# Kernel tuning notes

Measured on AMD Instinct MI355X. Metric: run time of the kernel, lower is better.

## Reference

```python
import jax, jax.numpy as jnp
import numpy as np

N_NODES = 50000
N_EDGES = 800000
HIDDEN = 128
EPS = 1e-5


def _layernorm(x, g, b):
    m = jnp.mean(x, axis=-1, keepdims=True)
    v = jnp.var(x, axis=-1, keepdims=True)
    return (x - m) / jnp.sqrt(v + EPS) * g + b


def _batchnorm(x, g, b):
    # training-mode BatchNorm1d: stats over the node (batch) axis, biased var
    m = jnp.mean(x, axis=0, keepdims=True)
    v = jnp.var(x, axis=0, keepdims=True)
    return (x - m) / jnp.sqrt(v + EPS) * g + b


def _instnorm(x):
    # torch InstanceNorm1d on a 2D [N,C] input: unbatched (C,L) view ->
    # normalize each row over the feature axis, no affine params
    m = jnp.mean(x, axis=-1, keepdims=True)
    v = jnp.var(x, axis=-1, keepdims=True)
    return (x - m) / jnp.sqrt(v + EPS)


def _gcn_conv(x, W, b, row, col, norm, n):
    # PyG GCNConv: out[col] += norm * (x @ W)[row]; + bias
    xw = x @ W
    msgs = xw[row] * norm[:, None]          # [E+N, H]
    out = jax.ops.segment_sum(msgs, col, num_segments=n)
    return out + b


def setup_inputs() -> dict:
    key = jax.random.key(0)
    ks = jax.random.split(key, 12)
    H = HIDDEN
    x = jax.random.normal(ks[0], (N_NODES, 2), dtype=jnp.float32)
    edge_index = jax.random.randint(ks[1], (2, N_EDGES), 0, N_NODES, dtype=jnp.int64)

    def lin(k, fan_in, shape):
        bound = 1.0 / np.sqrt(fan_in)
        return jax.random.uniform(k, shape, jnp.float32, -bound, bound)

    inp = {
        "x": x,
        "edge_index": edge_index,
        "coord_W": lin(ks[2], 2, (2, H)),
        "coord_b": lin(ks[3], 2, (H,)),
        "ln_g": jnp.ones((H,), jnp.float32),
        "ln_b": jnp.zeros((H,), jnp.float32),
        "bn_g": jnp.ones((H,), jnp.float32),
        "bn_b": jnp.zeros((H,), jnp.float32),
        "W1": lin(ks[4], H, (H, H)),
        "b1": jnp.zeros((H,), jnp.float32),
        "W2": lin(ks[5], H, (H, H)),
        "b2": jnp.zeros((H,), jnp.float32),
        "W3": lin(ks[6], H, (H, H)),
        "b3": jnp.zeros((H,), jnp.float32),
        "fc1_W": lin(ks[7], H, (H, 32)),
        "fc1_b": lin(ks[8], H, (32,)),
        "fc2_W": lin(ks[9], 32, (32, 2)),
        "fc2_b": lin(ks[10], 32, (2,)),
    }
    return inp


def reference(x, edge_index, coord_W, coord_b, ln_g, ln_b, bn_g, bn_b,
              W1, b1, W2, b2, W3, b3, fc1_W, fc1_b, fc2_W, fc2_b):
    n = x.shape[0]
    loop = jnp.arange(n, dtype=edge_index.dtype)
    row = jnp.concatenate([edge_index[0], loop])
    col = jnp.concatenate([edge_index[1], loop])
    deg = jax.ops.segment_sum(jnp.ones_like(col, dtype=x.dtype), col, num_segments=n)
    dinv = 1.0 / jnp.sqrt(deg)              # deg >= 1 thanks to self-loops
    norm = dinv[row] * dinv[col]

    h = jax.nn.relu(x @ coord_W + coord_b)
    h = _layernorm(h, ln_g, ln_b)

    for W, b in ((W1, b1), (W2, b2), (W3, b3)):
        identity = h
        h = jax.nn.relu(_gcn_conv(h, W, b, row, col, norm, n))
        h = _batchnorm(h, bn_g, bn_b)
        h = _instnorm(h + identity)

    h = jax.nn.relu(h @ fc1_W + fc1_b)
    return jnp.tanh(h @ fc2_W + fc2_b)
```

## Files before the change

kernel.cpp:

```cpp
#include <hip/hip_runtime.h>
#include <hip/hip_bf16.h>
#include <hip/hip_fp16.h>
#include <stdint.h>

#define NN 50000
#define NE 800000
#define HD 128
#define EPSN 1e-5f
#define CAP 1152000

typedef __hip_bfloat16 bf16;
typedef __attribute__((ext_vector_type(8))) _Float16 half8;
typedef __attribute__((ext_vector_type(4))) float f32x4;

__device__ __forceinline__ float us2f(unsigned short u) { return __uint_as_float((uint32_t)u << 16); }
__device__ __forceinline__ ushort f2us(float f) {
    bf16 b = __float2bfloat16(f);
    return *reinterpret_cast<ushort*>(&b);
}
__device__ __forceinline__ ushort f2h(float f) {
    __half h = __float2half(f);
    return *reinterpret_cast<ushort*>(&h);
}
__device__ __forceinline__ float h2f(ushort u) {
    __half h = *reinterpret_cast<__half*>(&u);
    return __half2float(h);
}

__device__ __forceinline__ void cvt8(float4 v, float* o) {
    uint32_t a = __float_as_uint(v.x), b = __float_as_uint(v.y);
    uint32_t c = __float_as_uint(v.z), d = __float_as_uint(v.w);
    o[0] = h2f((ushort)(a & 0xffff)); o[1] = h2f((ushort)(a >> 16));
    o[2] = h2f((ushort)(b & 0xffff)); o[3] = h2f((ushort)(b >> 16));
    o[4] = h2f((ushort)(c & 0xffff)); o[5] = h2f((ushort)(c >> 16));
    o[6] = h2f((ushort)(d & 0xffff)); o[7] = h2f((ushort)(d >> 16));
}

#define O_X    0
#define O_CW   100000
#define O_CB   100256
#define O_LNG  100384
#define O_LNB  100512
#define O_BNG  100640
#define O_BNB  100768
#define O_W1   100896
#define O_B1   117280
#define O_W2   117408
#define O_B2   133792
#define O_W3   133920
#define O_B3   150304
#define O_F1W  150432
#define O_F1B  154528
#define O_F2W  154560
#define O_F2B  154624
#define O_TOT  154626

struct Ptrs { const void* p[17]; };

__device__ const int SEG_OFF[18] = {O_X, O_CW, O_CB, O_LNG, O_LNB, O_BNG, O_BNB,
                                    O_W1, O_B1, O_W2, O_B2, O_W3, O_B3,
                                    O_F1W, O_F1B, O_F2W, O_F2B, O_TOT};

__device__ __forceinline__ int eidx(const int* __restrict__ ei, int isL, int which, int e) {
    size_t base = (size_t)which * NE + e;
    return isL ? ei[2 * base] : ei[base];
}

__global__ void k_detect(const int* __restrict__ ei, const ushort* __restrict__ cw,
                         int* __restrict__ flags) {
    int t = threadIdx.x;
    int v = ei[2 * t + 1] | ei[1000000 + 2 * t + 1];
    int bad = 0;
    if (t < 128) {
        float val = us2f(cw[2 * t]);
        bad = !(fabsf(val) <= 1.0f);
    }
    for (int o = 32; o; o >>= 1) { v |= __shfl_xor(v, o); bad |= __shfl_xor(bad, o); }
    __shared__ int sv[4], sb[4];
    if ((t & 63) == 0) { sv[t >> 6] = v; sb[t >> 6] = bad; }
    __syncthreads();
    if (t == 0) {
        flags[0] = ((sv[0] | sv[1] | sv[2] | sv[3]) == 0) ? 1 : 0;
        flags[1] = ((sb[0] | sb[1] | sb[2] | sb[3]) == 0) ? 1 : 0;
    }
}

__global__ void k_conv(Ptrs ptrs, const int* __restrict__ flags, float* __restrict__ cp) {
    int i = blockIdx.x * 256 + threadIdx.x;
    if (i >= O_TOT) return;
    int s = 0;
    while (i >= SEG_OFF[s + 1]) s++;
    int local = i - SEG_OFF[s];
    const void* src = ptrs.p[s];
    cp[i] = flags[1] ? us2f(((const ushort*)src)[local]) : ((const float*)src)[local];
}

__global__ void k_wconv(const float* __restrict__ cp, _Float16* __restrict__ wt) {
    int e = blockIdx.x * 256 + threadIdx.x;
    if (e >= 3 * HD * HD) return;
    int mat = e >> 14, idx = e & (HD * HD - 1);
    int k = idx >> 7, n = idx & 127;
    const float* W = cp + (mat == 0 ? O_W1 : (mat == 1 ? O_W2 : O_W3));
    wt[mat * HD * HD + n * HD + k] = (_Float16)W[k * HD + n];
}


__global__ void k_init(int* __restrict__ deg, float* __restrict__ stats,
                       int* __restrict__ cursor) {
    int i = blockIdx.x * 256 + threadIdx.x;
    if (i < NN) deg[i] = 1;
    if (i < 3072) stats[i] = 0.f;
    if (i == 0) *cursor = 0;
}

__global__ void k_deg(const int* __restrict__ ei, const int* __restrict__ flags,
                      int* __restrict__ deg) {
    int e = blockIdx.x * 256 + threadIdx.x;
    if (e < NE) atomicAdd(&deg[eidx(ei, flags[0], 1, e)], 1);
}

__global__ void k_dinv_alloc(const int* __restrict__ deg, float* __restrict__ dinv,
                             int* __restrict__ startA, int* __restrict__ curA,
                             int* __restrict__ cursor, int2* __restrict__ srw) {
    int i = blockIdx.x * 256 + threadIdx.x;
    if (i < NN) {
        int d = deg[i];
        dinv[i] = rsqrtf((float)d);
        int cnt = d - 1;
        int cpad = (cnt + 7) & ~7;
        int s = atomicAdd(cursor, cpad);
        startA[i] = s;
        curA[i] = s;
        for (int p = s + cnt; p < s + cpad; p++) srw[p] = make_int2(0, 0);
    }
}

__global__ void k_fill(const int* __restrict__ ei, const int* __restrict__ flags,
                       const float* __restrict__ dinv, int* __restrict__ curA,
                       int2* __restrict__ srw) {
    int e = blockIdx.x * 256 + threadIdx.x;
    if (e >= NE) return;
    int isL = flags[0];
    int r = eidx(ei, isL, 0, e);
    int c = eidx(ei, isL, 1, e);
    int p = atomicAdd(&curA[c], 1);
    srw[p] = make_int2(r << 4, __float_as_int(dinv[r] * dinv[c]));
}


__global__ void k_embed(const float* __restrict__ cp, float* __restrict__ h) {
    int node = (blockIdx.x * 256 + threadIdx.x) >> 6;
    int lane = threadIdx.x & 63;
    if (node >= NN) return;
    const float* X = cp + O_X;
    const float* CW = cp + O_CW;
    const float* CB = cp + O_CB;
    const float* LG = cp + O_LNG;
    const float* LB = cp + O_LNB;
    float x0 = X[node * 2], x1 = X[node * 2 + 1];
    int f0 = lane, f1 = lane + 64;
    float v0 = fmaxf(0.f, x0 * CW[f0] + x1 * CW[HD + f0] + CB[f0]);
    float v1 = fmaxf(0.f, x0 * CW[f1] + x1 * CW[HD + f1] + CB[f1]);
    float s = v0 + v1, q = v0 * v0 + v1 * v1;
    for (int o = 32; o; o >>= 1) { s += __shfl_xor(s, o); q += __shfl_xor(q, o); }
    float m = s * (1.f / HD);
    float var = q * (1.f / HD) - m * m;
    float r = rsqrtf(var + EPSN);
    h[(size_t)node * HD + f0] = (v0 - m) * r * LG[f0] + LB[f0];
    h[(size_t)node * HD + f1] = (v1 - m) * r * LG[f1] + LB[f1];
}


__device__ __forceinline__ void mfma_tile(const _Float16* hl, const _Float16* __restrict__ wt,
                                          ushort* __restrict__ t0h, int nodeBase, int t) {
    int w = t >> 6, l = t & 63;
    int m16 = l & 15;
    int kg = l >> 4;
    int node0 = w * 16;
    half8 a[4];
#pragma unroll
    for (int kc = 0; kc < 4; kc++) {
        int nd = node0 + m16;
        int c16 = kc * 4 + kg;
        int chunk = nd * 16 + (c16 ^ (nd & 7));
        a[kc] = *(const half8*)(hl + chunk * 8);
    }
    f32x4 acc[8];
#pragma unroll
    for (int nt = 0; nt < 8; nt++) acc[nt] = (f32x4){0.f, 0.f, 0.f, 0.f};
#pragma unroll
    for (int nt = 0; nt < 8; nt++) {
        const half8* bp = (const half8*)(wt + (size_t)(nt * 16 + m16) * HD);
#pragma unroll
        for (int kc = 0; kc < 4; kc++) {
            acc[nt] = __builtin_amdgcn_mfma_f32_16x16x32_f16(a[kc], bp[kc * 4 + kg],
                                                             acc[nt], 0, 0, 0);
        }
    }
    int ndb = nodeBase + node0 + kg * 4;
#pragma unroll
    for (int rr = 0; rr < 4; rr++) {
        int nd = ndb + rr;
        if (nd < NN) {
#pragma unroll
            for (int nt = 0; nt < 8; nt++) {
                t0h[(size_t)nd * HD + nt * 16 + m16] = f2h(acc[nt][rr]);
            }
        }
    }
}


__global__ __launch_bounds__(256) void k_gemm(const float* __restrict__ h,
                                              const _Float16* __restrict__ wt,
                                              ushort* __restrict__ t0h) {
    __shared__ _Float16 hl[64 * HD];
    int t = threadIdx.x;
    int nodeBase = blockIdx.x * 64;
    const float4* h4 = (const float4*)h;
#pragma unroll
    for (int r = 0; r < 4; r++) {
        int cid = r * 256 + t;
        int node = cid >> 4;
        int c16 = cid & 15;
        int n = nodeBase + node;
        float4 u0 = make_float4(0.f, 0.f, 0.f, 0.f), u1 = u0;
        if (n < NN) {
            u0 = h4[(size_t)n * 32 + c16 * 2];
            u1 = h4[(size_t)n * 32 + c16 * 2 + 1];
        }
        half8 v;
        v[0] = (_Float16)u0.x; v[1] = (_Float16)u0.y;
        v[2] = (_Float16)u0.z; v[3] = (_Float16)u0.w;
        v[4] = (_Float16)u1.x; v[5] = (_Float16)u1.y;
        v[6] = (_Float16)u1.z; v[7] = (_Float16)u1.w;
        int chunk = node * 16 + (c16 ^ (node & 7));
        *(half8*)(hl + chunk * 8) = v;
    }
    __syncthreads();
    mfma_tile(hl, wt, t0h, nodeBase, t);
}


__global__ __launch_bounds__(256) void k_gemm_fused(const float* __restrict__ agg,
                                                    const float* __restrict__ stats,
                                                    const float* __restrict__ bias,
                                                    const float* __restrict__ bng,
                                                    const float* __restrict__ bnb,
                                                    float* __restrict__ h,
                                                    const _Float16* __restrict__ wt,
                                                    ushort* __restrict__ t0h) {
    __shared__ _Float16 hl[64 * HD];
    __shared__ float scL[HD], shL[HD], bL[HD];
    int t = threadIdx.x;
    if (t < 128) {
        const float invN = 1.f / NN;
        float sv = stats[t] + stats[256 + t] + stats[512 + t] + stats[768 + t];
        float qv = stats[128 + t] + stats[384 + t] + stats[640 + t] + stats[896 + t];
        float m = sv * invN;
        float v = qv * invN - m * m;
        float sc = bng[t] * rsqrtf(v + EPSN);
        scL[t] = sc;
        shL[t] = bnb[t] - m * sc;
        bL[t] = bias[t];
    }
    __syncthreads();
    int nodeBase = blockIdx.x * 64;
    const float4* a4 = (const float4*)agg;
    float4* h4g = (float4*)h;
#pragma unroll
    for (int r = 0; r < 8; r++) {
        int idx = r * 256 + t;
        int node = idx >> 5;
        int c4 = idx & 31;
        int n = nodeBase + node;
        float4 u = make_float4(0.f, 0.f, 0.f, 0.f);
        if (n < NN) {
            float4 av = a4[(size_t)n * 32 + c4];
            float4 hv = h4g[(size_t)n * 32 + c4];
            int f = c4 * 4;
            float y0 = fmaxf(0.f, av.x + bL[f]);
            float y1 = fmaxf(0.f, av.y + bL[f + 1]);
            float y2 = fmaxf(0.f, av.z + bL[f + 2]);
            float y3 = fmaxf(0.f, av.w + bL[f + 3]);
            u.x = y0 * scL[f]     + shL[f]     + hv.x;
            u.y = y1 * scL[f + 1] + shL[f + 1] + hv.y;
            u.z = y2 * scL[f + 2] + shL[f + 2] + hv.z;
            u.w = y3 * scL[f + 3] + shL[f + 3] + hv.w;
        }
        float s = u.x + u.y + u.z + u.w;
        float q = u.x * u.x + u.y * u.y + u.z * u.z + u.w * u.w;
        for (int o = 16; o; o >>= 1) { s += __shfl_xor(s, o); q += __shfl_xor(q, o); }
        float m = s * (1.f / HD);
        float var = q * (1.f / HD) - m * m;
        float rr = rsqrtf(var + EPSN);
        u.x = (u.x - m) * rr; u.y = (u.y - m) * rr;
        u.z = (u.z - m) * rr; u.w = (u.w - m) * rr;
        if (n < NN) h4g[(size_t)n * 32 + c4] = u;
        ushort4 pk;
        pk.x = f2h(u.x); pk.y = f2h(u.y); pk.z = f2h(u.z); pk.w = f2h(u.w);
        int chunk = node * 16 + ((c4 >> 1) ^ (node & 7));
        *(ushort4*)((char*)hl + chunk * 16 + (c4 & 1) * 8) = pk;
    }
    __syncthreads();
    mfma_tile(hl, wt, t0h, nodeBase, t);
}


__global__ __launch_bounds__(256) void k_agg(const ushort* __restrict__ t0h,
                                             const int2* __restrict__ srw,
                                             const int* __restrict__ startA,
                                             const int* __restrict__ deg,
                                             const float* __restrict__ dinv,
                                             const float* __restrict__ bias,
                                             float* __restrict__ agg,
                                             float* __restrict__ stats) {
    int t = threadIdx.x;
    int w = t >> 6;
    int l = t & 63;
    int g = l >> 4;
    int k = l & 15;
    int l32 = l & 31;
    const float4* t04 = (const float4*)t0h;
    float4* agg4 = (float4*)agg;
    float bs[8];
    {
        const float4* b4 = (const float4*)bias;
        float4 u0 = b4[2 * k], u1 = b4[2 * k + 1];
        bs[0] = u0.x; bs[1] = u0.y; bs[2] = u0.z; bs[3] = u0.w;
        bs[4] = u1.x; bs[5] = u1.y; bs[6] = u1.z; bs[7] = u1.w;
    }
    float rs1[8], rs2[8];
#pragma unroll
    for (int m = 0; m < 8; m++) { rs1[m] = 0.f; rs2[m] = 0.f; }
    int stride = gridDim.x * 4;
    int i = blockIdx.x * 4 + w;
    int s = 0, nb = 0;
    float di = 0.f;
    if (i < NN) {
        s = startA[i];
        nb = (deg[i] - 1 + 7) & ~7;
        di = dinv[i];
    }
    while (i < NN) {
        float4 sv = t04[(size_t)i * 16 + k];
        int2 e = make_int2(0, 0);
        if (l32 < nb) e = srw[s + l32];
        int ex = e.x, ey = e.y;
        int nb4 = nb >> 2;
        float4 gg[8];
#define GATH(b) { int rv = __shfl(ex, 4 * (b) + g); \
                  gg[b] = t04[(size_t)(uint32_t)rv + k]; }
        if (nb4 > 0) { GATH(0) GATH(1) }
        if (nb4 > 2) { GATH(2) GATH(3) }
        if (nb4 > 4) { GATH(4) GATH(5) }
        if (nb4 > 6) { GATH(6) GATH(7) }
#undef GATH
        int inext = i + stride;
        int sN = 0, nbN = 0;
        float diN = 0.f;
        if (inext < NN) {
            sN = startA[inext];
            nbN = (deg[inext] - 1 + 7) & ~7;
            diN = dinv[inext];
        }
        float acc[8], c8[8];
        cvt8(sv, c8);
        float ws = (g == 0) ? di * di : 0.f;
#pragma unroll
        for (int m = 0; m < 8; m++) acc[m] = ws * c8[m];
#define ACCB(b) { float wv = __int_as_float(__shfl(ey, 4 * (b) + g)); \
                  float d8[8]; cvt8(gg[b], d8); \
                  _Pragma("unroll") \
                  for (int m = 0; m < 8; m++) acc[m] += wv * d8[m]; }
        if (nb4 > 0) { ACCB(0) ACCB(1) }
        if (nb4 > 2) { ACCB(2) ACCB(3) }
        if (nb4 > 4) { ACCB(4) ACCB(5) }
        if (nb4 > 6) { ACCB(6) ACCB(7) }
#undef ACCB
        for (int j = 32; j < nb; j += 32) {
            int2 e2 = make_int2(0, 0);
            if (j + l32 < nb) e2 = srw[s + j + l32];
            int ex2 = e2.x, ey2 = e2.y;
            int rem4 = (nb - j) >> 2;
            if (rem4 > 8) rem4 = 8;
            for (int b = 0; b < rem4; b += 2) {
                int r0 = __shfl(ex2, 4 * b + g);
                int r1 = __shfl(ex2, 4 * b + 4 + g);
                float4 g0 = t04[(size_t)(uint32_t)r0 + k];
                float4 g1 = t04[(size_t)(uint32_t)r1 + k];
                float w0 = __int_as_float(__shfl(ey2, 4 * b + g));
                float w1 = __int_as_float(__shfl(ey2, 4 * b + 4 + g));
                float d0[8], d1[8];
                cvt8(g0, d0); cvt8(g1, d1);
#pragma unroll
                for (int m = 0; m < 8; m++) acc[m] += w0 * d0[m] + w1 * d1[m];
            }
        }
#pragma unroll
        for (int m = 0; m < 8; m++) {
            acc[m] += __shfl_xor(acc[m], 16);
            acc[m] += __shfl_xor(acc[m], 32);
        }
        if (g == 0) {
            agg4[(size_t)i * 32 + 2 * k]     = make_float4(acc[0], acc[1], acc[2], acc[3]);
            agg4[(size_t)i * 32 + 2 * k + 1] = make_float4(acc[4], acc[5], acc[6], acc[7]);
        }
#pragma unroll
        for (int m = 0; m < 8; m++) {
            float y = fmaxf(0.f, acc[m] + bs[m]);
            rs1[m] += y;
            rs2[m] += y * y;
        }
        i = inext; s = sN; nb = nbN; di = diN;
    }
    __shared__ float s1[4][HD], s2[4][HD];
    if (l < 16) {
#pragma unroll
        for (int m = 0; m < 8; m++) {
            s1[w][k * 8 + m] = rs1[m];
            s2[w][k * 8 + m] = rs2[m];
        }
    }
    __syncthreads();
    float* st = stats + (blockIdx.x & 3) * 256;
    if (t < 128) {
        atomicAdd(&st[t], s1[0][t] + s1[1][t] + s1[2][t] + s1[3][t]);
    } else {
        int f = t - 128;
        atomicAdd(&st[128 + f], s2[0][f] + s2[1][f] + s2[2][f] + s2[3][f]);
    }
}


__global__ __launch_bounds__(256) void k_tail(const float* __restrict__ agg,
                                              const float* __restrict__ stats,
                                              const float* __restrict__ h,
                                              const float* __restrict__ cp,
                                              const int* __restrict__ flags,
                                              void* __restrict__ outv) {
    __shared__ float W1l[HD * 32];
    __shared__ float ub[4][HD];
    __shared__ float scT[HD], shT[HD], bT[HD];
    __shared__ float B1s[32], W2s[64], B2s[2];
    int t = threadIdx.x;
    const float4* f1w4 = (const float4*)(cp + O_F1W);
    float4* w14 = (float4*)W1l;
#pragma unroll
    for (int r = 0; r < 4; r++) w14[r * 256 + t] = f1w4[r * 256 + t];
    if (t < 32) B1s[t] = cp[O_F1B + t];
    if (t < 64) W2s[t] = cp[O_F2W + t];
    if (t < 2) B2s[t] = cp[O_F2B + t];
    if (t < 128) {
        const float invN = 1.f / NN;
        float sv = stats[t] + stats[256 + t] + stats[512 + t] + stats[768 + t];
        float qv = stats[128 + t] + stats[384 + t] + stats[640 + t] + stats[896 + t];
        float m = sv * invN;
        float v = qv * invN - m * m;
        float sc = cp[O_BNG + t] * rsqrtf(v + EPSN);
        scT[t] = sc;
        shT[t] = cp[O_BNB + t] - m * sc;
        bT[t] = cp[O_B3 + t];
    }
    __syncthreads();
    int isBf = flags[1];
    int w = t >> 6, l = t & 63;
    int f = l & 31, half = l >> 5;
    for (int base = blockIdx.x * 4; base < NN; base += gridDim.x * 4) {
        int node = base + w;
        if (node >= NN) continue;
        size_t o = (size_t)node * HD;
        float a0 = agg[o + l], a1 = agg[o + l + 64];
        float h0 = h[o + l],  h1 = h[o + l + 64];
        float y0 = fmaxf(0.f, a0 + bT[l]);
        float y1 = fmaxf(0.f, a1 + bT[l + 64]);
        float u0 = y0 * scT[l]      + shT[l]      + h0;
        float u1 = y1 * scT[l + 64] + shT[l + 64] + h1;
        float s = u0 + u1, q = u0 * u0 + u1 * u1;
        for (int oo = 32; oo; oo >>= 1) { s += __shfl_xor(s, oo); q += __shfl_xor(q, oo); }
        float m = s * (1.f / HD);
        float var = q * (1.f / HD) - m * m;
        float r = rsqrtf(var + EPSN);
        u0 = (u0 - m) * r; u1 = (u1 - m) * r;
        ub[w][l] = u0; ub[w][l + 64] = u1;
        float acc = (half == 0) ? B1s[f] : 0.f;
        const float* up = ub[w] + half * 64;
        const float* wp = W1l + half * 64 * 32 + f;
#pragma unroll 16
        for (int kk = 0; kk < 64; kk++) acc += up[kk] * wp[kk * 32];
        acc += __shfl_xor(acc, 32);
        float av = fmaxf(0.f, acc);
        float p0 = av * W2s[f * 2], p1 = av * W2s[f * 2 + 1];
        for (int oo = 16; oo; oo >>= 1) { p0 += __shfl_xor(p0, oo); p1 += __shfl_xor(p1, oo); }
        if (l == 0) {
            p0 = tanhf(p0 + B2s[0]); p1 = tanhf(p1 + B2s[1]);
            if (isBf) {
                ((uint32_t*)outv)[node] = (uint32_t)f2us(p0) | ((uint32_t)f2us(p1) << 16);
            } else {
                float2 ov; ov.x = p0; ov.y = p1;
                ((float2*)outv)[node] = ov;
            }
        }
    }
}


extern "C" void kernel_launch(void* const* d_in, const int* in_sizes, int n_in,
                              void* d_out, int out_size, void* d_ws, size_t ws_size,
                              hipStream_t stream) {
    const int* ei = (const int*)d_in[1];

    Ptrs ptrs;
    ptrs.p[0] = d_in[0];
    for (int s = 1; s < 17; s++) ptrs.p[s] = d_in[s + 1];

    char* wsp = (char*)d_ws;
    size_t off = 0;
    auto alloc = [&](size_t bytes) {
        void* p = wsp + off;
        off += (bytes + 255) & ~(size_t)255;
        return p;
    };
    float* cp     = (float*)alloc((size_t)O_TOT * 4);
    float* h      = (float*)alloc((size_t)NN * HD * 4);
    ushort* t0h   = (ushort*)alloc((size_t)NN * HD * 2);
    float* agg    = (float*)alloc((size_t)NN * HD * 4);
    int* deg      = (int*)alloc((size_t)NN * 4);
    float* dinv   = (float*)alloc((size_t)NN * 4);
    int2* srw     = (int2*)alloc((size_t)CAP * 8);
    int* startA   = (int*)alloc((size_t)NN * 4);
    int* curA     = (int*)alloc((size_t)NN * 4);
    float* stats  = (float*)alloc(3 * 1024 * 4);
    int* cursor   = (int*)alloc(256);
    int* flags    = (int*)alloc(256);
    _Float16* wt  = (_Float16*)alloc((size_t)3 * HD * HD * 2);

    const int BN_NODE = (NN + 255) / 256;
    const int BN_EDGE = (NE + 255) / 256;
    const int BN_CONV = (O_TOT + 255) / 256;
    const int BN_W    = (3 * HD * HD + 255) / 256;
    const int BN_GEMM = (NN + 63) / 64;

    const float* B[3] = {cp + O_B1, cp + O_B2, cp + O_B3};

    k_detect<<<1, 256, 0, stream>>>(ei, (const ushort*)d_in[2], flags);
    k_conv<<<BN_CONV, 256, 0, stream>>>(ptrs, flags, cp);
    k_wconv<<<BN_W, 256, 0, stream>>>(cp, wt);
    k_init<<<BN_NODE, 256, 0, stream>>>(deg, stats, cursor);
    k_deg<<<BN_EDGE, 256, 0, stream>>>(ei, flags, deg);
    k_dinv_alloc<<<BN_NODE, 256, 0, stream>>>(deg, dinv, startA, curA, cursor, srw);
    k_fill<<<BN_EDGE, 256, 0, stream>>>(ei, flags, dinv, curA, srw);
    k_embed<<<NN / 4, 256, 0, stream>>>(cp, h);

    k_gemm<<<BN_GEMM, 256, 0, stream>>>(h, wt, t0h);
    k_agg<<<1024, 256, 0, stream>>>(t0h, srw, startA, deg, dinv, B[0], agg, stats);
    for (int l = 1; l < 3; l++) {
        k_gemm_fused<<<BN_GEMM, 256, 0, stream>>>(agg, stats + 1024 * (l - 1),
                                                  B[l - 1], cp + O_BNG, cp + O_BNB,
                                                  h, wt + (size_t)l * HD * HD, t0h);
        k_agg<<<1024, 256, 0, stream>>>(t0h, srw, startA, deg, dinv, B[l],
                                        agg, stats + 1024 * l);
    }
    k_tail<<<1024, 256, 0, stream>>>(agg, stats + 2048, h, cp, flags, d_out);
}
```

Before: 502.6 us.

## Store residual hidden state in fp16 and widen agg/stat partitioning

The residual hidden-state buffer h goes from fp32 to fp16 across embed, gemm, gemm_fused and tail. This halves its memory traffic and lets k_gemm copy it into shared memory without conversion. The stats partial-sum slots go from 4 to 8 to reduce atomic contention, and the agg/tail grids double to 2048 blocks. Storing the residual in fp16 loses some precision.

```diff
diff --git a/kernel.cpp b/kernel.cpp
--- a/kernel.cpp
+++ b/kernel.cpp
@@ -109,7 +109,7 @@
                        int* __restrict__ cursor) {
     int i = blockIdx.x * 256 + threadIdx.x;
     if (i < NN) deg[i] = 1;
-    if (i < 3072) stats[i] = 0.f;
+    if (i < 6144) stats[i] = 0.f;
     if (i == 0) *cursor = 0;
 }
 
@@ -148,7 +148,7 @@
 }
 
 
-__global__ void k_embed(const float* __restrict__ cp, float* __restrict__ h) {
+__global__ void k_embed(const float* __restrict__ cp, ushort* __restrict__ h) {
     int node = (blockIdx.x * 256 + threadIdx.x) >> 6;
     int lane = threadIdx.x & 63;
     if (node >= NN) return;
@@ -166,8 +166,8 @@
     float m = s * (1.f / HD);
     float var = q * (1.f / HD) - m * m;
     float r = rsqrtf(var + EPSN);
-    h[(size_t)node * HD + f0] = (v0 - m) * r * LG[f0] + LB[f0];
-    h[(size_t)node * HD + f1] = (v1 - m) * r * LG[f1] + LB[f1];
+    h[(size_t)node * HD + f0] = f2h((v0 - m) * r * LG[f0] + LB[f0]);
+    h[(size_t)node * HD + f1] = f2h((v1 - m) * r * LG[f1] + LB[f1]);
 }
 
 
@@ -211,31 +211,23 @@
 }
 
 
-__global__ __launch_bounds__(256) void k_gemm(const float* __restrict__ h,
+__global__ __launch_bounds__(256) void k_gemm(const ushort* __restrict__ h,
                                               const _Float16* __restrict__ wt,
                                               ushort* __restrict__ t0h) {
     __shared__ _Float16 hl[64 * HD];
     int t = threadIdx.x;
     int nodeBase = blockIdx.x * 64;
-    const float4* h4 = (const float4*)h;
+    const uint4* h4 = (const uint4*)h;
 #pragma unroll
     for (int r = 0; r < 4; r++) {
         int cid = r * 256 + t;
         int node = cid >> 4;
         int c16 = cid & 15;
         int n = nodeBase + node;
-        float4 u0 = make_float4(0.f, 0.f, 0.f, 0.f), u1 = u0;
-        if (n < NN) {
-            u0 = h4[(size_t)n * 32 + c16 * 2];
-            u1 = h4[(size_t)n * 32 + c16 * 2 + 1];
-        }
-        half8 v;
-        v[0] = (_Float16)u0.x; v[1] = (_Float16)u0.y;
-        v[2] = (_Float16)u0.z; v[3] = (_Float16)u0.w;
-        v[4] = (_Float16)u1.x; v[5] = (_Float16)u1.y;
-        v[6] = (_Float16)u1.z; v[7] = (_Float16)u1.w;
+        uint4 v = make_uint4(0u, 0u, 0u, 0u);
+        if (n < NN) v = h4[(size_t)n * 16 + c16];
         int chunk = node * 16 + (c16 ^ (node & 7));
-        *(half8*)(hl + chunk * 8) = v;
+        *(uint4*)(hl + chunk * 8) = v;
     }
     __syncthreads();
     mfma_tile(hl, wt, t0h, nodeBase, t);
@@ -247,7 +239,7 @@
                                                     const float* __restrict__ bias,
                                                     const float* __restrict__ bng,
                                                     const float* __restrict__ bnb,
-                                                    float* __restrict__ h,
+                                                    ushort* __restrict__ h,
                                                     const _Float16* __restrict__ wt,
                                                     ushort* __restrict__ t0h) {
     __shared__ _Float16 hl[64 * HD];
@@ -255,8 +247,9 @@
     int t = threadIdx.x;
     if (t < 128) {
         const float invN = 1.f / NN;
-        float sv = stats[t] + stats[256 + t] + stats[512 + t] + stats[768 + t];
-        float qv = stats[128 + t] + stats[384 + t] + stats[640 + t] + stats[896 + t];
+        float sv = 0.f, qv = 0.f;
+#pragma unroll
+        for (int r = 0; r < 8; r++) { sv += stats[r * 256 + t]; qv += stats[r * 256 + 128 + t]; }
         float m = sv * invN;
         float v = qv * invN - m * m;
         float sc = bng[t] * rsqrtf(v + EPSN);
@@ -267,7 +260,8 @@
     __syncthreads();
     int nodeBase = blockIdx.x * 64;
     const float4* a4 = (const float4*)agg;
-    float4* h4g = (float4*)h;
+    const ushort4* h4r = (const ushort4*)h;
+    ushort4* h4w = (ushort4*)h;
 #pragma unroll
     for (int r = 0; r < 8; r++) {
         int idx = r * 256 + t;
@@ -277,16 +271,16 @@
         float4 u = make_float4(0.f, 0.f, 0.f, 0.f);
         if (n < NN) {
             float4 av = a4[(size_t)n * 32 + c4];
-            float4 hv = h4g[(size_t)n * 32 + c4];
+            ushort4 hv = h4r[(size_t)n * 32 + c4];
             int f = c4 * 4;
             float y0 = fmaxf(0.f, av.x + bL[f]);
             float y1 = fmaxf(0.f, av.y + bL[f + 1]);
             float y2 = fmaxf(0.f, av.z + bL[f + 2]);
             float y3 = fmaxf(0.f, av.w + bL[f + 3]);
-            u.x = y0 * scL[f]     + shL[f]     + hv.x;
-            u.y = y1 * scL[f + 1] + shL[f + 1] + hv.y;
-            u.z = y2 * scL[f + 2] + shL[f + 2] + hv.z;
-            u.w = y3 * scL[f + 3] + shL[f + 3] + hv.w;
+            u.x = y0 * scL[f]     + shL[f]     + h2f(hv.x);
+            u.y = y1 * scL[f + 1] + shL[f + 1] + h2f(hv.y);
+            u.z = y2 * scL[f + 2] + shL[f + 2] + h2f(hv.z);
+            u.w = y3 * scL[f + 3] + shL[f + 3] + h2f(hv.w);
         }
         float s = u.x + u.y + u.z + u.w;
         float q = u.x * u.x + u.y * u.y + u.z * u.z + u.w * u.w;
@@ -296,9 +290,9 @@
         float rr = rsqrtf(var + EPSN);
         u.x = (u.x - m) * rr; u.y = (u.y - m) * rr;
         u.z = (u.z - m) * rr; u.w = (u.w - m) * rr;
-        if (n < NN) h4g[(size_t)n * 32 + c4] = u;
         ushort4 pk;
         pk.x = f2h(u.x); pk.y = f2h(u.y); pk.z = f2h(u.z); pk.w = f2h(u.w);
+        if (n < NN) h4w[(size_t)n * 32 + c4] = pk;
         int chunk = node * 16 + ((c4 >> 1) ^ (node & 7));
         *(ushort4*)((char*)hl + chunk * 16 + (c4 & 1) * 8) = pk;
     }
@@ -423,7 +417,7 @@
         }
     }
     __syncthreads();
-    float* st = stats + (blockIdx.x & 3) * 256;
+    float* st = stats + (blockIdx.x & 7) * 256;
     if (t < 128) {
         atomicAdd(&st[t], s1[0][t] + s1[1][t] + s1[2][t] + s1[3][t]);
     } else {
@@ -435,7 +429,7 @@
 
 __global__ __launch_bounds__(256) void k_tail(const float* __restrict__ agg,
                                               const float* __restrict__ stats,
-                                              const float* __restrict__ h,
+                                              const ushort* __restrict__ h,
                                               const float* __restrict__ cp,
                                               const int* __restrict__ flags,
                                               void* __restrict__ outv) {
@@ -453,8 +447,9 @@
     if (t < 2) B2s[t] = cp[O_F2B + t];
     if (t < 128) {
         const float invN = 1.f / NN;
-        float sv = stats[t] + stats[256 + t] + stats[512 + t] + stats[768 + t];
-        float qv = stats[128 + t] + stats[384 + t] + stats[640 + t] + stats[896 + t];
+        float sv = 0.f, qv = 0.f;
+#pragma unroll
+        for (int r = 0; r < 8; r++) { sv += stats[r * 256 + t]; qv += stats[r * 256 + 128 + t]; }
         float m = sv * invN;
         float v = qv * invN - m * m;
         float sc = cp[O_BNG + t] * rsqrtf(v + EPSN);
@@ -471,7 +466,7 @@
         if (node >= NN) continue;
         size_t o = (size_t)node * HD;
         float a0 = agg[o + l], a1 = agg[o + l + 64];
-        float h0 = h[o + l],  h1 = h[o + l + 64];
+        float h0 = h2f(h[o + l]), h1 = h2f(h[o + l + 64]);
         float y0 = fmaxf(0.f, a0 + bT[l]);
         float y1 = fmaxf(0.f, a1 + bT[l + 64]);
         float u0 = y0 * scT[l]      + shT[l]      + h0;
@@ -522,7 +517,7 @@
         return p;
     };
     float* cp     = (float*)alloc((size_t)O_TOT * 4);
-    float* h      = (float*)alloc((size_t)NN * HD * 4);
+    ushort* h     = (ushort*)alloc((size_t)NN * HD * 2);
     ushort* t0h   = (ushort*)alloc((size_t)NN * HD * 2);
     float* agg    = (float*)alloc((size_t)NN * HD * 4);
     int* deg      = (int*)alloc((size_t)NN * 4);
@@ -530,7 +525,7 @@
     int2* srw     = (int2*)alloc((size_t)CAP * 8);
     int* startA   = (int*)alloc((size_t)NN * 4);
     int* curA     = (int*)alloc((size_t)NN * 4);
-    float* stats  = (float*)alloc(3 * 1024 * 4);
+    float* stats  = (float*)alloc(3 * 2048 * 4);
     int* cursor   = (int*)alloc(256);
     int* flags    = (int*)alloc(256);
     _Float16* wt  = (_Float16*)alloc((size_t)3 * HD * HD * 2);
@@ -553,13 +548,13 @@
     k_embed<<<NN / 4, 256, 0, stream>>>(cp, h);
 
     k_gemm<<<BN_GEMM, 256, 0, stream>>>(h, wt, t0h);
-    k_agg<<<1024, 256, 0, stream>>>(t0h, srw, startA, deg, dinv, B[0], agg, stats);
+    k_agg<<<2048, 256, 0, stream>>>(t0h, srw, startA, deg, dinv, B[0], agg, stats);
     for (int l = 1; l < 3; l++) {
-        k_gemm_fused<<<BN_GEMM, 256, 0, stream>>>(agg, stats + 1024 * (l - 1),
+        k_gemm_fused<<<BN_GEMM, 256, 0, stream>>>(agg, stats + 2048 * (l - 1),
                                                   B[l - 1], cp + O_BNG, cp + O_BNB,
                                                   h, wt + (size_t)l * HD * HD, t0h);
-        k_agg<<<1024, 256, 0, stream>>>(t0h, srw, startA, deg, dinv, B[l],
-                                        agg, stats + 1024 * l);
-    }
-    k_tail<<<1024, 256, 0, stream>>>(agg, stats + 2048, h, cp, flags, d_out);
-}
+        k_agg<<<2048, 256, 0, stream>>>(t0h, srw, startA, deg, dinv, B[l],
+                                        agg, stats + 2048 * l);
+    }
+    k_tail<<<2048, 256, 0, stream>>>(agg, stats + 4096, h, cp, flags, d_out);
+}
```

New measurement: 457.1 us. 1.1x faster.
